# Optimization experiments

Measured on AMD Instinct MI355X. Metric: run time of the kernel, lower is better.

Reference implementation:

```python
import jax, jax.numpy as jnp
import numpy as np

N_NODES = 20000
N_EDGES = 320000
N_GRAPHS = 64
D = 128  # node_dim


def _gat_conv(h, W, al, ar, b, src, dst, n, res=None, act=None):
    # DGL GATConv: fc -> per-head attn logits -> leaky_relu -> edge softmax per dst -> scatter-add
    H, Dh = al.shape
    feat = (h @ W).reshape(n, H, Dh)                      # [N,H,D]
    el = jnp.einsum('nhd,hd->nh', feat, al)               # [N,H]
    er = jnp.einsum('nhd,hd->nh', feat, ar)               # [N,H]
    e = jax.nn.leaky_relu(el[src] + er[dst], 0.2)         # [E,H]
    m = jax.ops.segment_max(e, dst, num_segments=n)       # [N,H]
    m = jnp.where(jnp.isfinite(m), m, 0.0)
    a = jnp.exp(e - m[dst])                               # [E,H]
    den = jax.ops.segment_sum(a, dst, num_segments=n)     # [N,H]
    a = a / jnp.maximum(den, 1e-9)[dst]
    out = jax.ops.segment_sum(a[:, :, None] * feat[src], dst, num_segments=n)  # [N,H,D]
    if res is not None:
        out = out + res
    out = out + b.reshape(1, H, Dh)
    return act(out) if act is not None else out


def setup_inputs() -> dict:
    key = jax.random.key(0)
    ks = jax.random.split(key, 20)
    s = 0.05
    inp = {
        'h': jax.random.normal(ks[0], (N_NODES, D), jnp.float32),
        'he': jax.random.normal(ks[1], (N_EDGES, 64), jnp.float32),
        'src': jax.random.randint(ks[2], (N_EDGES,), 0, N_NODES),
        'dst': jax.random.randint(ks[3], (N_EDGES,), 0, N_NODES),
        'graph_id': jnp.sort(jax.random.randint(ks[4], (N_NODES,), 0, N_GRAPHS)),
        # layer 0: in=D, heads=4, out=D
        'W0': jax.random.normal(ks[5], (D, 4 * D), jnp.float32) * s,
        'al0': jax.random.normal(ks[6], (4, D), jnp.float32) * s,
        'ar0': jax.random.normal(ks[7], (4, D), jnp.float32) * s,
        'b0': jnp.zeros((4 * D,), jnp.float32),
        # layer 1: in=4D, heads=4, out=D, residual (identity since 4D==4*D)
        'W1': jax.random.normal(ks[8], (4 * D, 4 * D), jnp.float32) * s,
        'al1': jax.random.normal(ks[9], (4, D), jnp.float32) * s,
        'ar1': jax.random.normal(ks[10], (4, D), jnp.float32) * s,
        'b1': jnp.zeros((4 * D,), jnp.float32),
        # layer 2: in=4D, heads=6, out=D, residual via res_fc (4D -> 6D)
        'W2': jax.random.normal(ks[11], (4 * D, 6 * D), jnp.float32) * s,
        'al2': jax.random.normal(ks[12], (6, D), jnp.float32) * s,
        'ar2': jax.random.normal(ks[13], (6, D), jnp.float32) * s,
        'b2': jnp.zeros((6 * D,), jnp.float32),
        'resW2': jax.random.normal(ks[14], (4 * D, 6 * D), jnp.float32) * s,
        # final MLP (1 layer): Linear(D, D)
        'Wm': jax.random.normal(ks[15], (D, D), jnp.float32) * s,
        'bm': jnp.zeros((D,), jnp.float32),
    }
    return inp


def reference(h, he, src, dst, graph_id, W0, al0, ar0, b0, W1, al1, ar1, b1,
              W2, al2, ar2, b2, resW2, Wm, bm):
    n = h.shape[0]
    elu = jax.nn.elu
    # layer 0 (no residual, elu), flatten heads
    x = _gat_conv(h, W0, al0, ar0, b0, src, dst, n, res=None, act=elu)
    x = x.reshape(n, -1)  # [N, 4D]
    # layer 1 (identity residual, elu), flatten heads
    res1 = x.reshape(n, 4, D)
    x2 = _gat_conv(x, W1, al1, ar1, b1, src, dst, n, res=res1, act=elu)
    x2 = x2.reshape(n, -1)  # [N, 4D]
    # layer 2 (linear residual, no activation), mean over heads
    res2 = (x2 @ resW2).reshape(n, 6, D)
    x3 = _gat_conv(x2, W2, al2, ar2, b2, src, dst, n, res=res2, act=None)
    local_feat = x3.mean(axis=1)  # [N, D]
    # avg pooling per graph + linear
    sums = jax.ops.segment_sum(local_feat, graph_id, num_segments=N_GRAPHS)
    cnts = jax.ops.segment_sum(jnp.ones((n,), local_feat.dtype), graph_id, num_segments=N_GRAPHS)
    pooled = sums / jnp.maximum(cnts, 1.0)[:, None]  # [G, D]
    global_feat = pooled @ Wm + bm
    return (local_feat, global_feat)
```

## Files before the change

### kernel.cpp

```cpp
#include <hip/hip_runtime.h>
#include <math.h>


typedef _Float16 f16;
typedef __attribute__((ext_vector_type(8))) _Float16 half8;
typedef __attribute__((ext_vector_type(4))) _Float16 half4;
typedef __attribute__((ext_vector_type(4))) float float4v;

union U16 { unsigned short u; _Float16 h; };

#define M_PAD 20096
#define CHSTRIDE ((size_t)M_PAD * 64)

__device__ inline void gload_lds16(const void* g, void* l) {
    __builtin_amdgcn_global_load_lds((const __attribute__((address_space(1))) unsigned*)g,
                                     (__attribute__((address_space(3))) unsigned*)l,
                                     16, 0, 0);
}


__global__ __launch_bounds__(256) void deg_kernel(const int* __restrict__ dst,
                                                  int* __restrict__ deg, int E) {
    int e = blockIdx.x * 256 + threadIdx.x;
    if (e < E) atomicAdd(&deg[dst[e]], 1);
}

__global__ __launch_bounds__(1024) void scan_kernel(const int* __restrict__ deg,
                                                    int* __restrict__ row_off, int n) {
    __shared__ int sums[1024];
    int t = threadIdx.x;
    int CH = (n + 1023) >> 10;
    int base = t * CH;
    int s = 0;
    for (int i = 0; i < CH; ++i) { int idx = base + i; if (idx < n) s += deg[idx]; }
    sums[t] = s;
    __syncthreads();
    for (int off = 1; off < 1024; off <<= 1) {
        int v = (t >= off) ? sums[t - off] : 0;
        __syncthreads();
        sums[t] += v;
        __syncthreads();
    }
    int run = (t == 0) ? 0 : sums[t - 1];
    for (int i = 0; i < CH; ++i) {
        int idx = base + i;
        if (idx < n) { row_off[idx] = run; run += deg[idx]; }
    }
    if (t == 1023) row_off[n] = run;
}

__global__ __launch_bounds__(256) void fill_kernel(const int* __restrict__ src,
                                                   const int* __restrict__ dst,
                                                   const int* __restrict__ row_off,
                                                   int* __restrict__ fill,
                                                   int* __restrict__ csr_src, int E) {
    int e = blockIdx.x * 256 + threadIdx.x;
    if (e < E) {
        int d = dst[e];
        int pos = row_off[d] + atomicAdd(&fill[d], 1);
        csr_src[pos] = src[e];
    }
}


__global__ __launch_bounds__(256) void cvt_pad_kernel(const float* __restrict__ x,
                                                      f16* __restrict__ y,
                                                      long n_valid, long n_total) {
    long i = ((long)blockIdx.x * 256 + threadIdx.x) * 4;
    if (i >= n_total) return;
    float4 v = make_float4(0.f, 0.f, 0.f, 0.f);
    if (i < n_valid) v = *(const float4*)&x[i];
    half4 o; o[0] = (f16)v.x; o[1] = (f16)v.y; o[2] = (f16)v.z; o[3] = (f16)v.w;
    *(half4*)&y[i] = o;
}

__global__ __launch_bounds__(256) void transpose_cvt_kernel(const float* __restrict__ W,
                                                            f16* __restrict__ Wt,
                                                            int K, int N) {
    __shared__ float tile[32][33];
    int n0 = blockIdx.x * 32, k0 = blockIdx.y * 32;
    int tx = threadIdx.x, ty = threadIdx.y;
#pragma unroll
    for (int i = 0; i < 32; i += 8)
        tile[ty + i][tx] = W[(size_t)(k0 + ty + i) * N + n0 + tx];
    __syncthreads();
#pragma unroll
    for (int i = 0; i < 32; i += 8)
        Wt[(size_t)(n0 + ty + i) * K + k0 + tx] = (f16)tile[tx][ty + i];
}


__global__ __launch_bounds__(256) void gemm16_kernel(const f16* __restrict__ A,
                                                     const f16* __restrict__ Bt,
                                                     f16* __restrict__ Cc,
                                                     f16* __restrict__ Cr,
                                                     const float* __restrict__ al,
                                                     const float* __restrict__ ar,
                                                     float* __restrict__ el8,
                                                     float* __restrict__ er8,
                                                     int N, int K, int nchunk,
                                                     int nheads, int nvalid) {
    __shared__ f16 As[128 * 32];
    __shared__ f16 Bs[128 * 32];
    __shared__ float elds[2][2][128];
    int t = threadIdx.x;
    int w = t >> 6;
    int l = t & 63;
    size_t bm = (size_t)blockIdx.y * 128;
    int bn = blockIdx.x * 128;
    int wm = (w & 1) * 64;
    int wn = (w >> 1) * 64;

    int srow = t >> 2;
    int scol = (t & 3) * 8;
    const f16* ag0 = A + (bm + srow) * K + scol;
    const f16* ag1 = A + (bm + 64 + srow) * K + scol;
    const f16* bg0 = Bt + (size_t)(bn + srow) * K + scol;
    const f16* bg1 = Bt + (size_t)(bn + 64 + srow) * K + scol;
    f16* al0 = As + t * 8;
    f16* al1 = As + 2048 + t * 8;
    f16* bl0 = Bs + t * 8;
    f16* bl1 = Bs + 2048 + t * 8;

    float4v acc[4][4];
#pragma unroll
    for (int i = 0; i < 4; ++i)
#pragma unroll
        for (int j = 0; j < 4; ++j) acc[i][j] = (float4v)(0.f);

    int ml = l & 15, q = l >> 4;
    const f16* ap = As + (wm + ml) * 32 + q * 8;
    const f16* bp = Bs + (wn + ml) * 32 + q * 8;

    for (int k0 = 0; k0 < K; k0 += 32) {
        gload_lds16(ag0 + k0, al0);
        gload_lds16(ag1 + k0, al1);
        gload_lds16(bg0 + k0, bl0);
        gload_lds16(bg1 + k0, bl1);
        __syncthreads();
        half8 af[4], bf[4];
#pragma unroll
        for (int mt = 0; mt < 4; ++mt) af[mt] = *(const half8*)(ap + mt * 16 * 32);
#pragma unroll
        for (int nt = 0; nt < 4; ++nt) bf[nt] = *(const half8*)(bp + nt * 16 * 32);
#pragma unroll
        for (int mt = 0; mt < 4; ++mt)
#pragma unroll
            for (int nt = 0; nt < 4; ++nt)
                acc[mt][nt] = __builtin_amdgcn_mfma_f32_16x16x32_f16(bf[nt], af[mt],
                                                                     acc[mt][nt], 0, 0, 0);
        __syncthreads();
    }
#pragma unroll
    for (int mt = 0; mt < 4; ++mt) {
        size_t row = bm + wm + mt * 16 + ml;
#pragma unroll
        for (int nt = 0; nt < 4; ++nt) {
            half4 hv;
#pragma unroll
            for (int r = 0; r < 4; ++r) hv[r] = (f16)acc[mt][nt][r];
            int col = bn + wn + nt * 16 + q * 4;
            if (col < nchunk) {
                *(half4*)&Cc[(size_t)(col >> 6) * CHSTRIDE + row * 64 + (col & 63)] = hv;
            } else {
                *(half4*)&Cr[row * (size_t)(N - nchunk) + (col - nchunk)] = hv;
            }
        }
    }
    if (al != nullptr && bn < nheads * 128) {
        int hh = bn >> 7;
        float4 a4[4], r4[4];
#pragma unroll
        for (int nt = 0; nt < 4; ++nt) {
            int ci = hh * 128 + wn + nt * 16 + q * 4;
            a4[nt] = *(const float4*)&al[ci];
            r4[nt] = *(const float4*)&ar[ci];
        }
        int wnidx = wn >> 6;
#pragma unroll
        for (int mt = 0; mt < 4; ++mt) {
            float ep = 0.f, rp = 0.f;
#pragma unroll
            for (int nt = 0; nt < 4; ++nt) {
                ep += acc[mt][nt][0] * a4[nt].x + acc[mt][nt][1] * a4[nt].y
                    + acc[mt][nt][2] * a4[nt].z + acc[mt][nt][3] * a4[nt].w;
                rp += acc[mt][nt][0] * r4[nt].x + acc[mt][nt][1] * r4[nt].y
                    + acc[mt][nt][2] * r4[nt].z + acc[mt][nt][3] * r4[nt].w;
            }
            ep += __shfl_xor(ep, 16, 64); ep += __shfl_xor(ep, 32, 64);
            rp += __shfl_xor(rp, 16, 64); rp += __shfl_xor(rp, 32, 64);
            if (q == 0) {
                elds[0][wnidx][wm + mt * 16 + ml] = ep;
                elds[1][wnidx][wm + mt * 16 + ml] = rp;
            }
        }
        __syncthreads();
        int row = t & 127, which = t >> 7;
        long gv = (long)bm + row;
        if (gv < nvalid) {
            float vs = elds[which][0][row] + elds[which][1][row];
            if (which == 0) el8[gv * 8 + hh] = vs;
            else            er8[gv * 8 + hh] = vs;
        }
    }
}


__global__ __launch_bounds__(256, 8) void edge_weight_kernel(
        const float* __restrict__ el8, const float* __restrict__ er8,
        const int* __restrict__ row_off, const int* __restrict__ csr_src,
        unsigned short* __restrict__ wexp, float* __restrict__ inv8,
        int H, int n, int E) {
    int wid = threadIdx.x >> 6, lane = threadIdx.x & 63;
    for (int v = blockIdx.x * 4 + wid; v < n; v += 8192) {
        float era[6];
#pragma unroll
        for (int h = 0; h < 6; ++h) era[h] = (h < H) ? er8[(size_t)v * 8 + h] : 0.f;
        int beg = row_off[v], end = row_off[v + 1];
        float lsum[6] = {0.f, 0.f, 0.f, 0.f, 0.f, 0.f};
        for (int pos = beg; pos < end; pos += 64) {
            int cnt = min(64, end - pos);
            int s_l = (lane < cnt) ? csr_src[pos + lane] : 0;
            float4 a = *(const float4*)&el8[(size_t)s_l * 8];
            float2 bq = *(const float2*)&el8[(size_t)s_l * 8 + 4];
            float ee[6] = {a.x, a.y, a.z, a.w, bq.x, bq.y};
#pragma unroll
            for (int h = 0; h < 6; ++h) {
                if (h < H) {
                    float lg = ee[h] + era[h];
                    lg = (lg >= 0.f) ? lg : 0.2f * lg;
                    float wv = __expf(lg);
                    if (lane >= cnt) wv = 0.f;
                    lsum[h] += wv;
                    if (lane < cnt) {
                        U16 uu; uu.h = (f16)wv;
                        wexp[(size_t)h * E + pos + lane] = uu.u;
                    }
                }
            }
        }
#pragma unroll
        for (int h = 0; h < 6; ++h)
#pragma unroll
            for (int off = 32; off >= 1; off >>= 1)
                lsum[h] += __shfl_xor(lsum[h], off, 64);
        if (lane == 0) {
#pragma unroll
            for (int h = 0; h < 6; ++h)
                if (h < H) inv8[(size_t)v * 8 + h] = 1.f / fmaxf(lsum[h], 1e-9f);
        }
    }
}


__device__ __forceinline__ void agg_chunk_body(
        const f16* __restrict__ fc, const unsigned short* __restrict__ wh,
        const float* __restrict__ inv8, int head,
        const int* __restrict__ row_off, const int* __restrict__ csr_src,
        const f16* __restrict__ res, const float* __restrict__ bias,
        f16* __restrict__ out16, float* __restrict__ out32,
        int n, int width, int act, int chunk,
        int wave_id, int wavestride, int lane) {
    int c = lane >> 3;
    int j = lane & 7;
    int coff = j * 8;
    int cb = chunk * 64 + coff;
    float4 bv0 = *(const float4*)&bias[cb];
    float4 bv1 = *(const float4*)&bias[cb + 4];
    int clbase = lane & 56;

    for (int v0 = wave_id * 8; v0 < n; v0 += wavestride * 8) {
        int v = v0 + c;
        bool valid = (v < n);
        int beg = 0, end = 0;
        if (valid) { beg = row_off[v]; end = row_off[v + 1]; }
        int rounds = end - beg;
        rounds = max(rounds, __shfl_xor(rounds, 8, 64));
        rounds = max(rounds, __shfl_xor(rounds, 16, 64));
        rounds = max(rounds, __shfl_xor(rounds, 32, 64));
        float acc[8] = {0.f, 0.f, 0.f, 0.f, 0.f, 0.f, 0.f, 0.f};
        int s_pf = 0, w_pf = 0;
        for (int r = 0; r < rounds; ++r) {
            if ((r & 7) == 0) {
                int pidx = beg + r + j;
                bool ok = pidx < end;
                s_pf = ok ? csr_src[pidx] : 0;
                w_pf = ok ? (int)wh[pidx] : 0;
            }
            int srcl = clbase + (r & 7);
            int s  = __shfl(s_pf, srcl, 64);
            int wi = __shfl(w_pf, srcl, 64);
            U16 uu; uu.u = (unsigned short)wi;
            float wv = (float)uu.h;
            half8 f = *(const half8*)&fc[(size_t)s * 64 + coff];
#pragma unroll
            for (int k = 0; k < 8; ++k) acc[k] += wv * (float)f[k];
        }
        if (valid) {
            float inv = inv8[(size_t)v * 8 + head];
            float ox[8];
#pragma unroll
            for (int k = 0; k < 8; ++k) ox[k] = acc[k] * inv;
            size_t base = (size_t)v * width + cb;
            if (res) {
                half8 rr = *(const half8*)&res[base];
#pragma unroll
                for (int k = 0; k < 8; ++k) ox[k] += (float)rr[k];
            }
            ox[0] += bv0.x; ox[1] += bv0.y; ox[2] += bv0.z; ox[3] += bv0.w;
            ox[4] += bv1.x; ox[5] += bv1.y; ox[6] += bv1.z; ox[7] += bv1.w;
            if (act) {
#pragma unroll
                for (int k = 0; k < 8; ++k)
                    ox[k] = (ox[k] > 0.f) ? ox[k] : expm1f(ox[k]);
            }
            if (out16) {
                half8 o;
#pragma unroll
                for (int k = 0; k < 8; ++k) o[k] = (f16)ox[k];
                *(half8*)&out16[base] = o;
            } else {
                *(float4*)&out32[base]     = make_float4(ox[0], ox[1], ox[2], ox[3]);
                *(float4*)&out32[base + 4] = make_float4(ox[4], ox[5], ox[6], ox[7]);
            }
        }
    }
}

__global__ __launch_bounds__(256, 8) void agg_chunk_kernel(
        const f16* __restrict__ featc, const unsigned short* __restrict__ wexp,
        const float* __restrict__ inv8,
        const int* __restrict__ row_off, const int* __restrict__ csr_src,
        const f16* __restrict__ res, const float* __restrict__ bias,
        f16* __restrict__ out16, float* __restrict__ out32,
        int n, int nchunks, int width, int E, int act) {
    int wid = threadIdx.x >> 6, lane = threadIdx.x & 63;
    int b = blockIdx.x;
    {
        int chunk = b & 7;
        agg_chunk_body(featc + (size_t)chunk * CHSTRIDE, wexp + (size_t)(chunk >> 1) * E,
                       inv8, chunk >> 1, row_off, csr_src, res, bias, out16, out32,
                       n, width, act, chunk, (b >> 3) * 4 + wid, 1024, lane);
    }
    if (nchunks > 8) {
        int chunk = 8 + (b & 3);
        if (chunk < nchunks)
            agg_chunk_body(featc + (size_t)chunk * CHSTRIDE, wexp + (size_t)(chunk >> 1) * E,
                           inv8, chunk >> 1, row_off, csr_src, res, bias, out16, out32,
                           n, width, act, chunk, (b >> 2) * 4 + wid, 2048, lane);
    }
}


__global__ __launch_bounds__(128) void seg_kernel(const int* __restrict__ gid,
                                                  int* __restrict__ gstart, int n) {
    int g = threadIdx.x;
    if (g > 64) return;
    int lo = 0, hi = n;
    while (lo < hi) {
        int mid = (lo + hi) >> 1;
        if (gid[mid] < g) lo = mid + 1; else hi = mid;
    }
    gstart[g] = lo;
}

__global__ __launch_bounds__(128) void mean_pool_kernel(const float* __restrict__ x3,
                                                        float* __restrict__ local, int n) {
    int v = blockIdx.x;
    int d = threadIdx.x;
    const float* p = x3 + (size_t)v * 768;
    float s = 0.f;
#pragma unroll
    for (int h = 0; h < 6; ++h) s += p[h * 128 + d];
    local[(size_t)v * 128 + d] = s * (1.f / 6.f);
}

__global__ __launch_bounds__(256) void graph_pool_kernel(const float* __restrict__ local,
                                                         const int* __restrict__ gstart,
                                                         float* __restrict__ pooled) {
    __shared__ float buf[128];
    int g = blockIdx.x;
    int t = threadIdx.x;
    int c = t & 127;
    int sub = t >> 7;
    int beg = gstart[g], end = gstart[g + 1];
    float s = 0.f;
    for (int v = beg + sub; v < end; v += 2) s += local[(size_t)v * 128 + c];
    if (sub == 1) buf[c] = s;
    __syncthreads();
    if (sub == 0) {
        float tot = s + buf[c];
        float cntf = fmaxf((float)(end - beg), 1.f);
        pooled[g * 128 + c] = tot / cntf;
    }
}

__global__ void final_mlp_kernel(const float* __restrict__ pooled,
                                 const float* __restrict__ Wm,
                                 const float* __restrict__ bm,
                                 float* __restrict__ gout) {
    int g = blockIdx.x;
    int j = threadIdx.x;
    __shared__ float p[128];
    p[j] = pooled[g * 128 + j];
    __syncthreads();
    float s = 0.f;
#pragma unroll 16
    for (int k = 0; k < 128; ++k) s += p[k] * Wm[k * 128 + j];
    gout[g * 128 + j] = s + bm[j];
}


extern "C" void kernel_launch(void* const* d_in, const int* in_sizes, int n_in,
                              void* d_out, int out_size, void* d_ws, size_t ws_size,
                              hipStream_t stream) {
    const float* h     = (const float*)d_in[0];
    const int*   src   = (const int*)d_in[2];
    const int*   dst   = (const int*)d_in[3];
    const int*   gid   = (const int*)d_in[4];
    const float* W0    = (const float*)d_in[5];
    const float* al0   = (const float*)d_in[6];
    const float* ar0   = (const float*)d_in[7];
    const float* b0    = (const float*)d_in[8];
    const float* W1    = (const float*)d_in[9];
    const float* al1   = (const float*)d_in[10];
    const float* ar1   = (const float*)d_in[11];
    const float* b1    = (const float*)d_in[12];
    const float* W2    = (const float*)d_in[13];
    const float* al2   = (const float*)d_in[14];
    const float* ar2   = (const float*)d_in[15];
    const float* b2    = (const float*)d_in[16];
    const float* resW2 = (const float*)d_in[17];
    const float* Wm    = (const float*)d_in[18];
    const float* bm    = (const float*)d_in[19];

    const int n = in_sizes[0] / 128;
    const int E = in_sizes[2];

    size_t off = 0;
    auto take = [&](size_t bytes) -> void* {
        void* p = (char*)d_ws + off;
        off = (off + bytes + 255) & ~(size_t)255;
        return p;
    };
    f16* h16     = (f16*)take((size_t)M_PAD * 128 * 2);
    f16* Wt0     = (f16*)take((size_t)512 * 128 * 2);
    f16* Wt1     = (f16*)take((size_t)512 * 512 * 2);
    f16* Wt2cat  = (f16*)take((size_t)1536 * 512 * 2);
    f16* featc   = (f16*)take((size_t)12 * CHSTRIDE * 2);
    f16* res2    = (f16*)take((size_t)M_PAD * 768 * 2);
    f16* x1_16   = (f16*)take((size_t)M_PAD * 512 * 2);
    f16* x2_16   = (f16*)take((size_t)M_PAD * 512 * 2);
    float* x3    = (float*)take((size_t)n * 768 * 4);
    unsigned short* wexp = (unsigned short*)take((size_t)6 * E * 2);
    float* inv8  = (float*)take((size_t)n * 8 * 4);
    float* el8   = (float*)take((size_t)n * 8 * 4);
    float* er8   = (float*)take((size_t)n * 8 * 4);
    int* deg     = (int*)take((size_t)n * 4);
    int* row_off = (int*)take((size_t)(n + 1) * 4);
    int* fillc   = (int*)take((size_t)n * 4);
    int* csr_src = (int*)take((size_t)E * 4);
    int* gstart  = (int*)take(65 * 4);
    float* pooled = (float*)take(64 * 128 * 4);

    float* out_local  = (float*)d_out;
    float* out_global = (float*)d_out + (size_t)n * 128;

    hipMemsetAsync(deg, 0, (size_t)n * 4, stream);
    hipMemsetAsync(fillc, 0, (size_t)n * 4, stream);
    hipMemsetAsync(x1_16 + (size_t)n * 512, 0, (size_t)(M_PAD - n) * 512 * 2, stream);
    hipMemsetAsync(x2_16 + (size_t)n * 512, 0, (size_t)(M_PAD - n) * 512 * 2, stream);

    {
        long nv = (long)n * 128, nt = (long)M_PAD * 128;
        cvt_pad_kernel<<<(int)((nt / 4 + 255) / 256), 256, 0, stream>>>(h, h16, nv, nt);
    }
    transpose_cvt_kernel<<<dim3(512 / 32, 128 / 32), dim3(32, 8), 0, stream>>>(W0, Wt0, 128, 512);
    transpose_cvt_kernel<<<dim3(512 / 32, 512 / 32), dim3(32, 8), 0, stream>>>(W1, Wt1, 512, 512);
    transpose_cvt_kernel<<<dim3(768 / 32, 512 / 32), dim3(32, 8), 0, stream>>>(W2, Wt2cat, 512, 768);
    transpose_cvt_kernel<<<dim3(768 / 32, 512 / 32), dim3(32, 8), 0, stream>>>(resW2, Wt2cat + (size_t)768 * 512, 512, 768);

    deg_kernel<<<(E + 255) / 256, 256, 0, stream>>>(dst, deg, E);
    scan_kernel<<<1, 1024, 0, stream>>>(deg, row_off, n);
    fill_kernel<<<(E + 255) / 256, 256, 0, stream>>>(src, dst, row_off, fillc, csr_src, E);
    seg_kernel<<<1, 128, 0, stream>>>(gid, gstart, n);

    const int gy = M_PAD / 128;

    gemm16_kernel<<<dim3(512 / 128, gy), 256, 0, stream>>>(h16, Wt0, featc, nullptr,
                                                           al0, ar0, el8, er8, 512, 128, 512, 4, n);
    edge_weight_kernel<<<2048, 256, 0, stream>>>(el8, er8, row_off, csr_src, wexp, inv8, 4, n, E);
    agg_chunk_kernel<<<2048, 256, 0, stream>>>(featc, wexp, inv8, row_off, csr_src,
                                               nullptr, b0, x1_16, nullptr, n, 8, 512, E, 1);
    gemm16_kernel<<<dim3(512 / 128, gy), 256, 0, stream>>>(x1_16, Wt1, featc, nullptr,
                                                           al1, ar1, el8, er8, 512, 512, 512, 4, n);
    edge_weight_kernel<<<2048, 256, 0, stream>>>(el8, er8, row_off, csr_src, wexp, inv8, 4, n, E);
    agg_chunk_kernel<<<2048, 256, 0, stream>>>(featc, wexp, inv8, row_off, csr_src,
                                               x1_16, b1, x2_16, nullptr, n, 8, 512, E, 1);
    gemm16_kernel<<<dim3(1536 / 128, gy), 256, 0, stream>>>(x2_16, Wt2cat, featc, res2,
                                                            al2, ar2, el8, er8, 1536, 512, 768, 6, n);
    edge_weight_kernel<<<2048, 256, 0, stream>>>(el8, er8, row_off, csr_src, wexp, inv8, 6, n, E);
    agg_chunk_kernel<<<2048, 256, 0, stream>>>(featc, wexp, inv8, row_off, csr_src,
                                               res2, b2, nullptr, x3, n, 12, 768, E, 0);
    mean_pool_kernel<<<n, 128, 0, stream>>>(x3, out_local, n);
    graph_pool_kernel<<<64, 256, 0, stream>>>(out_local, gstart, pooled);
    final_mlp_kernel<<<64, 128, 0, stream>>>(pooled, Wm, bm, out_global);
}
```

Measured before the change: 595.1 us.

## Reorganize GEMM LDS layout, shrink edge-weight lanes, merge small setup kernels

Changes the GEMM shared-memory tile layout to a k-quarter-major arrangement, likely to reduce LDS bank conflicts on the MFMA fragment reads. Edge-weight kernel now assigns 16 lanes per destination node instead of a full wavefront, matching the average degree of about 16 and cutting idle lanes. Also folds the graph-segment search into the scan kernel, merges two memsets, and replaces padding memsets with a zeroing kernel to cut launch count. The new GEMM layout must match the global_load_lds write order. Nodes with high degree now loop more within a 16-lane group.

```diff
diff --git a/kernel.cpp b/kernel.cpp
--- a/kernel.cpp
+++ b/kernel.cpp
@@ -26,9 +26,19 @@
 }
 
 __global__ __launch_bounds__(1024) void scan_kernel(const int* __restrict__ deg,
-                                                    int* __restrict__ row_off, int n) {
+                                                    int* __restrict__ row_off,
+                                                    const int* __restrict__ gid,
+                                                    int* __restrict__ gstart, int n) {
     __shared__ int sums[1024];
     int t = threadIdx.x;
+    if (t <= 64) {
+        int g = t, lo = 0, hi = n;
+        while (lo < hi) {
+            int mid = (lo + hi) >> 1;
+            if (gid[mid] < g) lo = mid + 1; else hi = mid;
+        }
+        gstart[g] = lo;
+    }
     int CH = (n + 1023) >> 10;
     int base = t * CH;
     int s = 0;
@@ -72,6 +82,17 @@
     if (i < n_valid) v = *(const float4*)&x[i];
     half4 o; o[0] = (f16)v.x; o[1] = (f16)v.y; o[2] = (f16)v.z; o[3] = (f16)v.w;
     *(half4*)&y[i] = o;
+}
+
+__global__ __launch_bounds__(256) void zero_pad_kernel(f16* __restrict__ x1,
+                                                       f16* __restrict__ x2, int n) {
+    int total = (M_PAD - n) * 512;
+    int idx = (blockIdx.x * 256 + threadIdx.x) * 4;
+    if (idx < total) {
+        half4 z; z[0] = (f16)0.f; z[1] = (f16)0.f; z[2] = (f16)0.f; z[3] = (f16)0.f;
+        *(half4*)&x1[(size_t)n * 512 + idx] = z;
+        *(half4*)&x2[(size_t)n * 512 + idx] = z;
+    }
 }
 
 __global__ __launch_bounds__(256) void transpose_cvt_kernel(const float* __restrict__ W,
@@ -111,12 +132,12 @@
     int wm = (w & 1) * 64;
     int wn = (w >> 1) * 64;
 
-    int srow = t >> 2;
-    int scol = (t & 3) * 8;
-    const f16* ag0 = A + (bm + srow) * K + scol;
-    const f16* ag1 = A + (bm + 64 + srow) * K + scol;
-    const f16* bg0 = Bt + (size_t)(bn + srow) * K + scol;
-    const f16* bg1 = Bt + (size_t)(bn + 64 + srow) * K + scol;
+    int row_s = t & 127;
+    int q0 = t >> 7;
+    const f16* ag0 = A + (bm + row_s) * K + q0 * 8;
+    const f16* ag1 = ag0 + 16;
+    const f16* bg0 = Bt + (size_t)(bn + row_s) * K + q0 * 8;
+    const f16* bg1 = bg0 + 16;
     f16* al0 = As + t * 8;
     f16* al1 = As + 2048 + t * 8;
     f16* bl0 = Bs + t * 8;
@@ -129,8 +150,8 @@
         for (int j = 0; j < 4; ++j) acc[i][j] = (float4v)(0.f);
 
     int ml = l & 15, q = l >> 4;
-    const f16* ap = As + (wm + ml) * 32 + q * 8;
-    const f16* bp = Bs + (wn + ml) * 32 + q * 8;
+    const f16* ap = As + q * 1024 + (wm + ml) * 8;
+    const f16* bp = Bs + q * 1024 + (wn + ml) * 8;
 
     for (int k0 = 0; k0 < K; k0 += 32) {
         gload_lds16(ag0 + k0, al0);
@@ -140,9 +161,9 @@
         __syncthreads();
         half8 af[4], bf[4];
 #pragma unroll
-        for (int mt = 0; mt < 4; ++mt) af[mt] = *(const half8*)(ap + mt * 16 * 32);
-#pragma unroll
-        for (int nt = 0; nt < 4; ++nt) bf[nt] = *(const half8*)(bp + nt * 16 * 32);
+        for (int mt = 0; mt < 4; ++mt) af[mt] = *(const half8*)(ap + mt * 128);
+#pragma unroll
+        for (int nt = 0; nt < 4; ++nt) bf[nt] = *(const half8*)(bp + nt * 128);
 #pragma unroll
         for (int mt = 0; mt < 4; ++mt)
 #pragma unroll
@@ -212,43 +233,49 @@
         unsigned short* __restrict__ wexp, float* __restrict__ inv8,
         int H, int n, int E) {
     int wid = threadIdx.x >> 6, lane = threadIdx.x & 63;
-    for (int v = blockIdx.x * 4 + wid; v < n; v += 8192) {
-        float era[6];
-#pragma unroll
-        for (int h = 0; h < 6; ++h) era[h] = (h < H) ? er8[(size_t)v * 8 + h] : 0.f;
-        int beg = row_off[v], end = row_off[v + 1];
-        float lsum[6] = {0.f, 0.f, 0.f, 0.f, 0.f, 0.f};
-        for (int pos = beg; pos < end; pos += 64) {
-            int cnt = min(64, end - pos);
-            int s_l = (lane < cnt) ? csr_src[pos + lane] : 0;
-            float4 a = *(const float4*)&el8[(size_t)s_l * 8];
-            float2 bq = *(const float2*)&el8[(size_t)s_l * 8 + 4];
-            float ee[6] = {a.x, a.y, a.z, a.w, bq.x, bq.y};
-#pragma unroll
-            for (int h = 0; h < 6; ++h) {
-                if (h < H) {
-                    float lg = ee[h] + era[h];
-                    lg = (lg >= 0.f) ? lg : 0.2f * lg;
-                    float wv = __expf(lg);
-                    if (lane >= cnt) wv = 0.f;
-                    lsum[h] += wv;
-                    if (lane < cnt) {
-                        U16 uu; uu.h = (f16)wv;
-                        wexp[(size_t)h * E + pos + lane] = uu.u;
-                    }
+    int c2 = lane >> 4;
+    int sl = lane & 15;
+    int v = blockIdx.x * 16 + wid * 4 + c2;
+    if (v >= n) return;
+    float era[6];
+    {
+        float4 a = *(const float4*)&er8[(size_t)v * 8];
+        float2 b = *(const float2*)&er8[(size_t)v * 8 + 4];
+        era[0] = a.x; era[1] = a.y; era[2] = a.z; era[3] = a.w;
+        era[4] = b.x; era[5] = b.y;
+    }
+    int beg = row_off[v], end = row_off[v + 1];
+    float lsum[6] = {0.f, 0.f, 0.f, 0.f, 0.f, 0.f};
+    for (int pos = beg; pos < end; pos += 16) {
+        int cnt = min(16, end - pos);
+        int s_l = (sl < cnt) ? csr_src[pos + sl] : 0;
+        float4 a = *(const float4*)&el8[(size_t)s_l * 8];
+        float2 bq = *(const float2*)&el8[(size_t)s_l * 8 + 4];
+        float ee[6] = {a.x, a.y, a.z, a.w, bq.x, bq.y};
+#pragma unroll
+        for (int h = 0; h < 6; ++h) {
+            if (h < H) {
+                float lg = ee[h] + era[h];
+                lg = (lg >= 0.f) ? lg : 0.2f * lg;
+                float wv = __expf(lg);
+                if (sl >= cnt) wv = 0.f;
+                lsum[h] += wv;
+                if (sl < cnt) {
+                    U16 uu; uu.h = (f16)wv;
+                    wexp[(size_t)h * E + pos + sl] = uu.u;
                 }
             }
         }
+    }
+#pragma unroll
+    for (int h = 0; h < 6; ++h)
+#pragma unroll
+        for (int off = 8; off >= 1; off >>= 1)
+            lsum[h] += __shfl_xor(lsum[h], off, 64);
+    if (sl == 0) {
 #pragma unroll
         for (int h = 0; h < 6; ++h)
-#pragma unroll
-            for (int off = 32; off >= 1; off >>= 1)
-                lsum[h] += __shfl_xor(lsum[h], off, 64);
-        if (lane == 0) {
-#pragma unroll
-            for (int h = 0; h < 6; ++h)
-                if (h < H) inv8[(size_t)v * 8 + h] = 1.f / fmaxf(lsum[h], 1e-9f);
-        }
+            if (h < H) inv8[(size_t)v * 8 + h] = 1.f / fmaxf(lsum[h], 1e-9f);
     }
 }
 
@@ -351,18 +378,6 @@
     }
 }
 
-
-__global__ __launch_bounds__(128) void seg_kernel(const int* __restrict__ gid,
-                                                  int* __restrict__ gstart, int n) {
-    int g = threadIdx.x;
-    if (g > 64) return;
-    int lo = 0, hi = n;
-    while (lo < hi) {
-        int mid = (lo + hi) >> 1;
-        if (gid[mid] < g) lo = mid + 1; else hi = mid;
-    }
-    gstart[g] = lo;
-}
 
 __global__ __launch_bounds__(128) void mean_pool_kernel(const float* __restrict__ x3,
                                                         float* __restrict__ local, int n) {
@@ -456,9 +471,9 @@
     float* inv8  = (float*)take((size_t)n * 8 * 4);
     float* el8   = (float*)take((size_t)n * 8 * 4);
     float* er8   = (float*)take((size_t)n * 8 * 4);
-    int* deg     = (int*)take((size_t)n * 4);
+    int* deg     = (int*)take((size_t)2 * n * 4);
+    int* fillc   = deg + n;
     int* row_off = (int*)take((size_t)(n + 1) * 4);
-    int* fillc   = (int*)take((size_t)n * 4);
     int* csr_src = (int*)take((size_t)E * 4);
     int* gstart  = (int*)take(65 * 4);
     float* pooled = (float*)take(64 * 128 * 4);
@@ -466,10 +481,8 @@
     float* out_local  = (float*)d_out;
     float* out_global = (float*)d_out + (size_t)n * 128;
 
-    hipMemsetAsync(deg, 0, (size_t)n * 4, stream);
-    hipMemsetAsync(fillc, 0, (size_t)n * 4, stream);
-    hipMemsetAsync(x1_16 + (size_t)n * 512, 0, (size_t)(M_PAD - n) * 512 * 2, stream);
-    hipMemsetAsync(x2_16 + (size_t)n * 512, 0, (size_t)(M_PAD - n) * 512 * 2, stream);
+    hipMemsetAsync(deg, 0, (size_t)2 * n * 4, stream);
+    zero_pad_kernel<<<(int)(((size_t)(M_PAD - n) * 512 / 4 + 255) / 256), 256, 0, stream>>>(x1_16, x2_16, n);
 
     {
         long nv = (long)n * 128, nt = (long)M_PAD * 128;
@@ -481,25 +494,25 @@
     transpose_cvt_kernel<<<dim3(768 / 32, 512 / 32), dim3(32, 8), 0, stream>>>(resW2, Wt2cat + (size_t)768 * 512, 512, 768);
 
     deg_kernel<<<(E + 255) / 256, 256, 0, stream>>>(dst, deg, E);
-    scan_kernel<<<1, 1024, 0, stream>>>(deg, row_off, n);
+    scan_kernel<<<1, 1024, 0, stream>>>(deg, row_off, gid, gstart, n);
     fill_kernel<<<(E + 255) / 256, 256, 0, stream>>>(src, dst, row_off, fillc, csr_src, E);
-    seg_kernel<<<1, 128, 0, stream>>>(gid, gstart, n);
 
     const int gy = M_PAD / 128;
+    const int ew_blocks = (n + 15) / 16;
 
     gemm16_kernel<<<dim3(512 / 128, gy), 256, 0, stream>>>(h16, Wt0, featc, nullptr,
                                                            al0, ar0, el8, er8, 512, 128, 512, 4, n);
-    edge_weight_kernel<<<2048, 256, 0, stream>>>(el8, er8, row_off, csr_src, wexp, inv8, 4, n, E);
+    edge_weight_kernel<<<ew_blocks, 256, 0, stream>>>(el8, er8, row_off, csr_src, wexp, inv8, 4, n, E);
     agg_chunk_kernel<<<2048, 256, 0, stream>>>(featc, wexp, inv8, row_off, csr_src,
                                                nullptr, b0, x1_16, nullptr, n, 8, 512, E, 1);
     gemm16_kernel<<<dim3(512 / 128, gy), 256, 0, stream>>>(x1_16, Wt1, featc, nullptr,
                                                            al1, ar1, el8, er8, 512, 512, 512, 4, n);
-    edge_weight_kernel<<<2048, 256, 0, stream>>>(el8, er8, row_off, csr_src, wexp, inv8, 4, n, E);
+    edge_weight_kernel<<<ew_blocks, 256, 0, stream>>>(el8, er8, row_off, csr_src, wexp, inv8, 4, n, E);
     agg_chunk_kernel<<<2048, 256, 0, stream>>>(featc, wexp, inv8, row_off, csr_src,
                                                x1_16, b1, x2_16, nullptr, n, 8, 512, E, 1);
     gemm16_kernel<<<dim3(1536 / 128, gy), 256, 0, stream>>>(x2_16, Wt2cat, featc, res2,
                                                             al2, ar2, el8, er8, 1536, 512, 768, 6, n);
-    edge_weight_kernel<<<2048, 256, 0, stream>>>(el8, er8, row_off, csr_src, wexp, inv8, 6, n, E);
+    edge_weight_kernel<<<ew_blocks, 256, 0, stream>>>(el8, er8, row_off, csr_src, wexp, inv8, 6, n, E);
     agg_chunk_kernel<<<2048, 256, 0, stream>>>(featc, wexp, inv8, row_off, csr_src,
                                                res2, b2, nullptr, x3, n, 12, 768, E, 0);
     mean_pool_kernel<<<n, 128, 0, stream>>>(x3, out_local, n);
```

New measurement: 595.3 us. Within noise of the previous version (+0.0%).
